# Performance work log

Measured on AMD Instinct MI355X. Metric: run time of the kernel, lower is better.

Reference implementation:

```python
import jax, jax.numpy as jnp
import numpy as np


def setup_inputs() -> dict:
    key = jax.random.key(0)
    kx, kw = jax.random.split(key)
    B, IN, OUT = 8192, 256, 16384
    x = jax.random.normal(kx, (B, IN), dtype=jnp.float32)
    weight = jax.random.normal(kw, (OUT, IN), dtype=jnp.float32)
    return {"x": x, "weight": weight}


def reference(x, weight):
    # Pairwise Euclidean distance ||x_b - w_o||_2 via expansion:
    temperature = 2.0
    x2 = jnp.sum(x * x, axis=1, keepdims=True)          # [B, 1]
    w2 = jnp.sum(weight * weight, axis=1)[None, :]       # [1, OUT]
    xw = x @ weight.T                                    # [B, OUT]
    d2 = jnp.maximum(x2 + w2 - 2.0 * xw, 0.0)            # clamp fp error
    dist = jnp.sqrt(d2)                                  # [B, OUT]
    return jax.nn.softmax(-temperature * dist, axis=1)
```

## Files before the change

kernel.cpp:

```cpp
#include <hip/hip_runtime.h>
#include <math.h>
#include <stdint.h>

#define M_ROWS 8192
#define N_COLS 16384
#define K_DIM  256
#define NTILE  (N_COLS / 128)
#define CHUNK  2048
#define NCHUNK 4

typedef _Float16 half8  __attribute__((ext_vector_type(8)));
typedef _Float16 half4v __attribute__((ext_vector_type(4)));
typedef float    vf4    __attribute__((ext_vector_type(4)));

__device__ __forceinline__ void gload16(const void* g, void* lds) {
  __builtin_amdgcn_global_load_lds(
      (__attribute__((address_space(1))) void*)(void*)g,
      (__attribute__((address_space(3))) void*)lds, 16, 0, 0);
}

__global__ __launch_bounds__(256) void prep_kernel(
    const float* __restrict__ x, const float* __restrict__ w,
    float* __restrict__ x2, float* __restrict__ w2,
    _Float16* __restrict__ xh, _Float16* __restrict__ wh) {
  int row  = blockIdx.x * 4 + (threadIdx.x >> 6);
  int lane = threadIdx.x & 63;
  const float* src; _Float16* dst; float* nrm;
  if (row < M_ROWS) {
    src = x + (size_t)row * K_DIM; dst = xh + (size_t)row * K_DIM; nrm = x2 + row;
  } else {
    int r = row - M_ROWS;
    src = w + (size_t)r * K_DIM; dst = wh + (size_t)r * K_DIM; nrm = w2 + r;
  }
  float4 v = ((const float4*)src)[lane];
  float s = v.x*v.x + v.y*v.y + v.z*v.z + v.w*v.w;
  #pragma unroll
  for (int off = 32; off > 0; off >>= 1) s += __shfl_down(s, off);
  if (lane == 0) *nrm = s;
  half4v h; h[0]=(_Float16)v.x; h[1]=(_Float16)v.y; h[2]=(_Float16)v.z; h[3]=(_Float16)v.w;
  ((half4v*)dst)[lane] = h;
}

template <int MODE>
__global__ __launch_bounds__(256, 3) void gemm_pass(
    const _Float16* __restrict__ A, const _Float16* __restrict__ Bm,
    const float* __restrict__ x2g, const float* __restrict__ w2g,
    const float* __restrict__ invg,
    float* __restrict__ partials,
    float* __restrict__ out) {
  __shared__ _Float16 As[128 * 64];
  __shared__ _Float16 Bs[128 * 64];
  __shared__ float x2s[128];
  __shared__ float w2s[128];
  __shared__ float invs[128];
  __shared__ float rowpart[2][128];

  int id   = blockIdx.x;
  int xcd  = id & 7;
  int rest = id >> 3;
  int ct   = xcd * 16 + (rest & 15);
  int rt   = rest >> 4;
  int brow = rt * 128;
  int bcol = ct * 128;

  int tid = threadIdx.x, lane = tid & 63, wid = tid >> 6;
  int wr = wid >> 1, wc = wid & 1;

  if (tid < 128) {
    x2s[tid] = x2g[brow + tid];
    if (MODE == 1) invs[tid] = invg[brow + tid];
  } else {
    w2s[tid - 128] = w2g[bcol + tid - 128];
  }

  vf4 acc[4][4] = {};

  for (int kk = 0; kk < K_DIM; kk += 64) {
    #pragma unroll
    for (int i = 0; i < 4; ++i) {
      int seg = wid * 4 + i;
      int r   = seg * 8 + (lane >> 3);
      int colhalf = ((lane & 7) * 8) ^ ((lane >> 3) << 3);
      gload16(A  + (size_t)(brow + r) * K_DIM + kk + colhalf, (char*)As + seg * 1024);
      gload16(Bm + (size_t)(bcol + r) * K_DIM + kk + colhalf, (char*)Bs + seg * 1024);
    }
    __syncthreads();

    #pragma unroll
    for (int ks = 0; ks < 2; ++ks) {
      half8 af[4], bf[4];
      int cb = ks * 64 + (lane >> 4) * 16;
      #pragma unroll
      for (int m = 0; m < 4; ++m) {
        int ra = wr * 64 + m * 16 + (lane & 15);
        af[m] = *(const half8*)((const char*)As + ra * 128 + (cb ^ ((ra & 7) << 4)));
      }
      #pragma unroll
      for (int n = 0; n < 4; ++n) {
        int rb = wc * 64 + n * 16 + (lane & 15);
        bf[n] = *(const half8*)((const char*)Bs + rb * 128 + (cb ^ ((rb & 7) << 4)));
      }
      #pragma unroll
      for (int m = 0; m < 4; ++m)
        #pragma unroll
        for (int n = 0; n < 4; ++n)
          acc[m][n] = __builtin_amdgcn_mfma_f32_16x16x32_f16(af[m], bf[n], acc[m][n], 0, 0, 0);
    }
    __syncthreads();
  }

  if (MODE == 0) {
    #pragma unroll
    for (int m = 0; m < 4; ++m) {
      #pragma unroll
      for (int j = 0; j < 4; ++j) {
        int rl = wr * 64 + m * 16 + ((lane >> 4) << 2) + j;
        float x2v = x2s[rl];
        float sm = 0.f;
        #pragma unroll
        for (int n = 0; n < 4; ++n) {
          int cl = wc * 64 + n * 16 + (lane & 15);
          float d2 = fmaxf(x2v + w2s[cl] - 2.0f * acc[m][n][j], 0.0f);
          sm += __expf(-2.0f * sqrtf(d2));
        }
        sm += __shfl_xor(sm, 1);
        sm += __shfl_xor(sm, 2);
        sm += __shfl_xor(sm, 4);
        sm += __shfl_xor(sm, 8);
        if ((lane & 15) == 0) rowpart[wc][rl] = sm;
      }
    }
    __syncthreads();
    if (tid < 128)
      partials[(size_t)(brow + tid) * NTILE + ct] = rowpart[0][tid] + rowpart[1][tid];
  } else {
    #pragma unroll
    for (int m = 0; m < 4; ++m) {
      #pragma unroll
      for (int j = 0; j < 4; ++j) {
        int rl = wr * 64 + m * 16 + ((lane >> 4) << 2) + j;
        float x2v = x2s[rl];
        float inv = invs[rl];
        size_t rowbase = (size_t)(brow + rl) * N_COLS + bcol;
        #pragma unroll
        for (int n = 0; n < 4; ++n) {
          int cl = wc * 64 + n * 16 + (lane & 15);
          float d2 = fmaxf(x2v + w2s[cl] - 2.0f * acc[m][n][j], 0.0f);
          out[rowbase + cl] = __expf(-2.0f * sqrtf(d2)) * inv;
        }
      }
    }
  }
}

__global__ __launch_bounds__(256) void reduce_inv(
    const float* __restrict__ partials, float* __restrict__ invg) {
  int row  = blockIdx.x * 4 + (threadIdx.x >> 6);
  int lane = threadIdx.x & 63;
  const float* p = partials + (size_t)row * NTILE;
  float s = p[lane] + p[lane + 64];
  #pragma unroll
  for (int off = 32; off > 0; off >>= 1) s += __shfl_down(s, off);
  if (lane == 0) invg[row] = 1.0f / s;
}

__global__ __launch_bounds__(256, 2) void gemm_logit_f32(
    const float* __restrict__ xf, const float* __restrict__ wf,
    float* __restrict__ out, int mbase) {
  __shared__ _Float16 As[128 * 64];
  __shared__ _Float16 Bs[128 * 64];
  __shared__ float x2s[128];
  __shared__ float w2s[128];

  int id  = blockIdx.x;
  int xcd = id & 7;
  int rt  = (id >> 3) & 15;
  int c2  = id >> 7;
  int brow = mbase + rt * 128;
  int bcol = (xcd * 16 + c2) * 128;

  int tid = threadIdx.x, lane = tid & 63, wid = tid >> 6;
  int wr = wid >> 1, wc = wid & 1;

  vf4 acc[4][4] = {};

  {
    const float* src = (tid < 128) ? xf + (size_t)(brow + tid) * K_DIM
                                   : wf + (size_t)(bcol + tid - 128) * K_DIM;
    float s = 0.f;
    for (int i = 0; i < 64; ++i) {
      float4 v = ((const float4*)src)[i];
      s += v.x*v.x + v.y*v.y + v.z*v.z + v.w*v.w;
    }
    if (tid < 128) x2s[tid] = s; else w2s[tid - 128] = s;
  }

  for (int kk = 0; kk < K_DIM; kk += 64) {
    #pragma unroll
    for (int i = 0; i < 8; ++i) {
      int idx = i * 256 + tid;
      int r = idx >> 4, kq = idx & 15;
      float4 va = ((const float4*)(xf + (size_t)(brow + r) * K_DIM + kk))[kq];
      float4 vb = ((const float4*)(wf + (size_t)(bcol + r) * K_DIM + kk))[kq];
      half4v ha; ha[0]=(_Float16)va.x; ha[1]=(_Float16)va.y; ha[2]=(_Float16)va.z; ha[3]=(_Float16)va.w;
      half4v hb; hb[0]=(_Float16)vb.x; hb[1]=(_Float16)vb.y; hb[2]=(_Float16)vb.z; hb[3]=(_Float16)vb.w;
      *(half4v*)&As[r * 64 + kq * 4] = ha;
      *(half4v*)&Bs[r * 64 + kq * 4] = hb;
    }
    __syncthreads();
    #pragma unroll
    for (int ks = 0; ks < 2; ++ks) {
      half8 af[4], bf[4];
      #pragma unroll
      for (int m = 0; m < 4; ++m)
        af[m] = *(const half8*)&As[(wr*64 + m*16 + (lane & 15)) * 64 + ks*32 + (lane >> 4) * 8];
      #pragma unroll
      for (int n = 0; n < 4; ++n)
        bf[n] = *(const half8*)&Bs[(wc*64 + n*16 + (lane & 15)) * 64 + ks*32 + (lane >> 4) * 8];
      #pragma unroll
      for (int m = 0; m < 4; ++m)
        #pragma unroll
        for (int n = 0; n < 4; ++n)
          acc[m][n] = __builtin_amdgcn_mfma_f32_16x16x32_f16(af[m], bf[n], acc[m][n], 0, 0, 0);
    }
    __syncthreads();
  }

  #pragma unroll
  for (int m = 0; m < 4; ++m) {
    int rl = wr * 64 + m * 16 + ((lane >> 4) << 2);
    #pragma unroll
    for (int n = 0; n < 4; ++n) {
      int cl = wc * 64 + n * 16 + (lane & 15);
      int c  = bcol + cl;
      float w2v = w2s[cl];
      #pragma unroll
      for (int j = 0; j < 4; ++j) {
        int r = brow + rl + j;
        float d2 = fmaxf(x2s[rl + j] + w2v - 2.0f * acc[m][n][j], 0.0f);
        out[(size_t)r * N_COLS + c] = -2.0f * sqrtf(d2);
      }
    }
  }
}

__global__ __launch_bounds__(256) void softmax_norm(float* __restrict__ io, int mbase) {
  int row = mbase + blockIdx.x;
  float* p = io + (size_t)row * N_COLS;
  int tid = threadIdx.x;
  __shared__ float wsum[4];

  float4 v[16];
  float s = 0.f;
  #pragma unroll
  for (int i = 0; i < 16; ++i) {
    v[i] = ((const float4*)p)[i * 256 + tid];
    v[i].x = __expf(v[i].x); v[i].y = __expf(v[i].y);
    v[i].z = __expf(v[i].z); v[i].w = __expf(v[i].w);
    s += v[i].x + v[i].y + v[i].z + v[i].w;
  }
  #pragma unroll
  for (int off = 32; off > 0; off >>= 1) s += __shfl_down(s, off);
  if ((tid & 63) == 0) wsum[tid >> 6] = s;
  __syncthreads();
  float inv = 1.0f / (wsum[0] + wsum[1] + wsum[2] + wsum[3]);
  #pragma unroll
  for (int i = 0; i < 16; ++i) {
    float4 o = v[i];
    o.x *= inv; o.y *= inv; o.z *= inv; o.w *= inv;
    ((float4*)p)[i * 256 + tid] = o;
  }
}

extern "C" void kernel_launch(void* const* d_in, const int* in_sizes, int n_in,
                              void* d_out, int out_size, void* d_ws, size_t ws_size,
                              hipStream_t stream) {
  const float* x = (const float*)d_in[0];
  const float* w = (const float*)d_in[1];
  float* out = (float*)d_out;

  char* ws = (char*)d_ws;
  float* x2 = (float*)ws;
  float* w2 = x2 + M_ROWS;
  float* invsum = w2 + N_COLS;
  float* partials = invsum + M_ROWS;
  _Float16* xh = (_Float16*)(partials + (size_t)M_ROWS * NTILE);
  _Float16* wh = xh + (size_t)M_ROWS * K_DIM;
  const size_t need = ((size_t)(M_ROWS + N_COLS + M_ROWS) + (size_t)M_ROWS * NTILE) * 4
                    + (size_t)(M_ROWS + N_COLS) * K_DIM * 2;

  if (ws_size >= need) {
    prep_kernel<<<(M_ROWS + N_COLS) / 4, 256, 0, stream>>>(x, w, x2, w2, xh, wh);
    gemm_pass<0><<<(M_ROWS / 128) * (N_COLS / 128), 256, 0, stream>>>(
        xh, wh, x2, w2, nullptr, partials, nullptr);
    reduce_inv<<<M_ROWS / 4, 256, 0, stream>>>(partials, invsum);
    gemm_pass<1><<<(M_ROWS / 128) * (N_COLS / 128), 256, 0, stream>>>(
        xh, wh, x2, w2, invsum, nullptr, out);
  } else {
    for (int c = 0; c < NCHUNK; ++c) {
      int mbase = c * CHUNK;
      gemm_logit_f32<<<(CHUNK / 128) * (N_COLS / 128), 256, 0, stream>>>(
          x, w, out, mbase);
      softmax_norm<<<CHUNK, 256, 0, stream>>>(out, mbase);
    }
  }
}
```

Baseline: 311.0 us.

## Pre-pack fp16 operands into MFMA fragment order and load directly to registers

The prep kernel now writes x and weight in fp16, arranged in 16-row by 32-k fragment blocks that match the MFMA operand layout. Each lane of the GEMM kernels can then load its half8 fragment straight from global memory, so the LDS staging, swizzling and __syncthreads barriers go away. The norms and inverse sums are also read from global memory instead of being staged in shared memory. The cost is that fragments are no longer shared through LDS, so each wave issues its own global loads and data reuse relies on L1/L2 caching.

```diff
diff --git a/kernel.cpp b/kernel.cpp
--- a/kernel.cpp
+++ b/kernel.cpp
@@ -13,46 +13,45 @@
 typedef _Float16 half4v __attribute__((ext_vector_type(4)));
 typedef float    vf4    __attribute__((ext_vector_type(4)));
 
-__device__ __forceinline__ void gload16(const void* g, void* lds) {
-  __builtin_amdgcn_global_load_lds(
-      (__attribute__((address_space(1))) void*)(void*)g,
-      (__attribute__((address_space(3))) void*)lds, 16, 0, 0);
-}
-
-__global__ __launch_bounds__(256) void prep_kernel(
+__global__ __launch_bounds__(256) void prep_pack(
     const float* __restrict__ x, const float* __restrict__ w,
     float* __restrict__ x2, float* __restrict__ w2,
-    _Float16* __restrict__ xh, _Float16* __restrict__ wh) {
-  int row  = blockIdx.x * 4 + (threadIdx.x >> 6);
+    _Float16* __restrict__ xp, _Float16* __restrict__ wp) {
+  int g    = blockIdx.x * 4 + (threadIdx.x >> 6);
   int lane = threadIdx.x & 63;
   const float* src; _Float16* dst; float* nrm;
-  if (row < M_ROWS) {
-    src = x + (size_t)row * K_DIM; dst = xh + (size_t)row * K_DIM; nrm = x2 + row;
+  if (g < M_ROWS / 16) {
+    src = x + (size_t)g * 16 * K_DIM; dst = xp + (size_t)g * 8 * 512; nrm = x2 + g * 16;
   } else {
-    int r = row - M_ROWS;
-    src = w + (size_t)r * K_DIM; dst = wh + (size_t)r * K_DIM; nrm = w2 + r;
-  }
-  float4 v = ((const float4*)src)[lane];
-  float s = v.x*v.x + v.y*v.y + v.z*v.z + v.w*v.w;
-  #pragma unroll
-  for (int off = 32; off > 0; off >>= 1) s += __shfl_down(s, off);
-  if (lane == 0) *nrm = s;
-  half4v h; h[0]=(_Float16)v.x; h[1]=(_Float16)v.y; h[2]=(_Float16)v.z; h[3]=(_Float16)v.w;
-  ((half4v*)dst)[lane] = h;
+    int g2 = g - M_ROWS / 16;
+    src = w + (size_t)g2 * 16 * K_DIM; dst = wp + (size_t)g2 * 8 * 512; nrm = w2 + g2 * 16;
+  }
+  int rowl = lane & 15, kpart = lane >> 4;
+  float ss = 0.f;
+  #pragma unroll
+  for (int S = 0; S < 8; ++S) {
+    const float* p = src + rowl * K_DIM + S * 32 + kpart * 8;
+    float4 a = *(const float4*)p;
+    float4 b = *(const float4*)(p + 4);
+    ss += a.x*a.x + a.y*a.y + a.z*a.z + a.w*a.w
+        + b.x*b.x + b.y*b.y + b.z*b.z + b.w*b.w;
+    half8 h;
+    h[0]=(_Float16)a.x; h[1]=(_Float16)a.y; h[2]=(_Float16)a.z; h[3]=(_Float16)a.w;
+    h[4]=(_Float16)b.x; h[5]=(_Float16)b.y; h[6]=(_Float16)b.z; h[7]=(_Float16)b.w;
+    *(half8*)(dst + S * 512 + lane * 8) = h;
+  }
+  ss += __shfl_xor(ss, 16);
+  ss += __shfl_xor(ss, 32);
+  if (lane < 16) nrm[lane] = ss;
 }
 
 template <int MODE>
 __global__ __launch_bounds__(256, 3) void gemm_pass(
-    const _Float16* __restrict__ A, const _Float16* __restrict__ Bm,
+    const _Float16* __restrict__ Ap, const _Float16* __restrict__ Bp,
     const float* __restrict__ x2g, const float* __restrict__ w2g,
     const float* __restrict__ invg,
     float* __restrict__ partials,
     float* __restrict__ out) {
-  __shared__ _Float16 As[128 * 64];
-  __shared__ _Float16 Bs[128 * 64];
-  __shared__ float x2s[128];
-  __shared__ float w2s[128];
-  __shared__ float invs[128];
   __shared__ float rowpart[2][128];
 
   int id   = blockIdx.x;
@@ -66,47 +65,25 @@
   int tid = threadIdx.x, lane = tid & 63, wid = tid >> 6;
   int wr = wid >> 1, wc = wid & 1;
 
-  if (tid < 128) {
-    x2s[tid] = x2g[brow + tid];
-    if (MODE == 1) invs[tid] = invg[brow + tid];
-  } else {
-    w2s[tid - 128] = w2g[bcol + tid - 128];
-  }
+  int RA = rt * 8 + wr * 4;
+  int RB = ct * 8 + wc * 4;
 
   vf4 acc[4][4] = {};
 
-  for (int kk = 0; kk < K_DIM; kk += 64) {
-    #pragma unroll
-    for (int i = 0; i < 4; ++i) {
-      int seg = wid * 4 + i;
-      int r   = seg * 8 + (lane >> 3);
-      int colhalf = ((lane & 7) * 8) ^ ((lane >> 3) << 3);
-      gload16(A  + (size_t)(brow + r) * K_DIM + kk + colhalf, (char*)As + seg * 1024);
-      gload16(Bm + (size_t)(bcol + r) * K_DIM + kk + colhalf, (char*)Bs + seg * 1024);
-    }
-    __syncthreads();
-
-    #pragma unroll
-    for (int ks = 0; ks < 2; ++ks) {
-      half8 af[4], bf[4];
-      int cb = ks * 64 + (lane >> 4) * 16;
-      #pragma unroll
-      for (int m = 0; m < 4; ++m) {
-        int ra = wr * 64 + m * 16 + (lane & 15);
-        af[m] = *(const half8*)((const char*)As + ra * 128 + (cb ^ ((ra & 7) << 4)));
-      }
-      #pragma unroll
-      for (int n = 0; n < 4; ++n) {
-        int rb = wc * 64 + n * 16 + (lane & 15);
-        bf[n] = *(const half8*)((const char*)Bs + rb * 128 + (cb ^ ((rb & 7) << 4)));
-      }
-      #pragma unroll
-      for (int m = 0; m < 4; ++m)
-        #pragma unroll
-        for (int n = 0; n < 4; ++n)
-          acc[m][n] = __builtin_amdgcn_mfma_f32_16x16x32_f16(af[m], bf[n], acc[m][n], 0, 0, 0);
-    }
-    __syncthreads();
+  #pragma unroll
+  for (int S = 0; S < 8; ++S) {
+    half8 af[4], bf[4];
+    #pragma unroll
+    for (int m = 0; m < 4; ++m)
+      af[m] = *(const half8*)(Ap + (((size_t)(RA + m) * 8 + S) << 9) + lane * 8);
+    #pragma unroll
+    for (int n = 0; n < 4; ++n)
+      bf[n] = *(const half8*)(Bp + (((size_t)(RB + n) * 8 + S) << 9) + lane * 8);
+    #pragma unroll
+    for (int m = 0; m < 4; ++m)
+      #pragma unroll
+      for (int n = 0; n < 4; ++n)
+        acc[m][n] = __builtin_amdgcn_mfma_f32_16x16x32_f16(af[m], bf[n], acc[m][n], 0, 0, 0);
   }
 
   if (MODE == 0) {
@@ -115,12 +92,12 @@
       #pragma unroll
       for (int j = 0; j < 4; ++j) {
         int rl = wr * 64 + m * 16 + ((lane >> 4) << 2) + j;
-        float x2v = x2s[rl];
+        float x2v = x2g[brow + rl];
         float sm = 0.f;
         #pragma unroll
         for (int n = 0; n < 4; ++n) {
           int cl = wc * 64 + n * 16 + (lane & 15);
-          float d2 = fmaxf(x2v + w2s[cl] - 2.0f * acc[m][n][j], 0.0f);
+          float d2 = fmaxf(x2v + w2g[bcol + cl] - 2.0f * acc[m][n][j], 0.0f);
           sm += __expf(-2.0f * sqrtf(d2));
         }
         sm += __shfl_xor(sm, 1);
@@ -139,13 +116,13 @@
       #pragma unroll
       for (int j = 0; j < 4; ++j) {
         int rl = wr * 64 + m * 16 + ((lane >> 4) << 2) + j;
-        float x2v = x2s[rl];
-        float inv = invs[rl];
+        float x2v = x2g[brow + rl];
+        float inv = invg[brow + rl];
         size_t rowbase = (size_t)(brow + rl) * N_COLS + bcol;
         #pragma unroll
         for (int n = 0; n < 4; ++n) {
           int cl = wc * 64 + n * 16 + (lane & 15);
-          float d2 = fmaxf(x2v + w2s[cl] - 2.0f * acc[m][n][j], 0.0f);
+          float d2 = fmaxf(x2v + w2g[bcol + cl] - 2.0f * acc[m][n][j], 0.0f);
           out[rowbase + cl] = __expf(-2.0f * sqrtf(d2)) * inv;
         }
       }
@@ -284,18 +261,18 @@
   float* w2 = x2 + M_ROWS;
   float* invsum = w2 + N_COLS;
   float* partials = invsum + M_ROWS;
-  _Float16* xh = (_Float16*)(partials + (size_t)M_ROWS * NTILE);
-  _Float16* wh = xh + (size_t)M_ROWS * K_DIM;
+  _Float16* xp = (_Float16*)(partials + (size_t)M_ROWS * NTILE);
+  _Float16* wp = xp + (size_t)M_ROWS * K_DIM;
   const size_t need = ((size_t)(M_ROWS + N_COLS + M_ROWS) + (size_t)M_ROWS * NTILE) * 4
                     + (size_t)(M_ROWS + N_COLS) * K_DIM * 2;
 
   if (ws_size >= need) {
-    prep_kernel<<<(M_ROWS + N_COLS) / 4, 256, 0, stream>>>(x, w, x2, w2, xh, wh);
+    prep_pack<<<(M_ROWS + N_COLS) / 16 / 4, 256, 0, stream>>>(x, w, x2, w2, xp, wp);
     gemm_pass<0><<<(M_ROWS / 128) * (N_COLS / 128), 256, 0, stream>>>(
-        xh, wh, x2, w2, nullptr, partials, nullptr);
+        xp, wp, x2, w2, nullptr, partials, nullptr);
     reduce_inv<<<M_ROWS / 4, 256, 0, stream>>>(partials, invsum);
     gemm_pass<1><<<(M_ROWS / 128) * (N_COLS / 128), 256, 0, stream>>>(
-        xh, wh, x2, w2, invsum, nullptr, out);
+        xp, wp, x2, w2, invsum, nullptr, out);
   } else {
     for (int c = 0; c < NCHUNK; ++c) {
       int mbase = c * CHUNK;
```

Result: slower. 384.3 us (+23.6%).

## Replace double GEMM pass with single GEMM storing fp16 dot products per chunk

Applied to the files above, without the earlier changes.

Instead of running the GEMM twice (once for row sums, once for output), each 2048-row chunk now runs the GEMM once. It writes fp16 dot products to a workspace buffer along with per-tile exp partial sums, then reduces and runs a streaming finalize kernel that recomputes distances and writes normalized outputs. This trades recomputed MFMA work for extra memory traffic through the intermediate buffer, which chunking may keep cache-resident. The old fp32 fallback path is removed.

```diff
diff --git a/kernel.cpp b/kernel.cpp
--- a/kernel.cpp
+++ b/kernel.cpp
@@ -6,8 +6,8 @@
 #define N_COLS 16384
 #define K_DIM  256
 #define NTILE  (N_COLS / 128)
-#define CHUNK  2048
-#define NCHUNK 4
+#define CROWS  2048
+#define NCHUNK (M_ROWS / CROWS)
 
 typedef _Float16 half8  __attribute__((ext_vector_type(8)));
 typedef _Float16 half4v __attribute__((ext_vector_type(4)));
@@ -39,6 +39,136 @@
   if (lane == 0) *nrm = s;
   half4v h; h[0]=(_Float16)v.x; h[1]=(_Float16)v.y; h[2]=(_Float16)v.z; h[3]=(_Float16)v.w;
   ((half4v*)dst)[lane] = h;
+}
+
+__global__ __launch_bounds__(256, 3) void gemm_xw(
+    const _Float16* __restrict__ A, const _Float16* __restrict__ Bm,
+    const float* __restrict__ x2g, const float* __restrict__ w2g,
+    float* __restrict__ partials, _Float16* __restrict__ xwc, int mbase) {
+  __shared__ _Float16 As[128 * 64];
+  __shared__ _Float16 Bs[128 * 64];
+  __shared__ float x2s[128];
+  __shared__ float w2s[128];
+  __shared__ float rowpart[2][128];
+
+  int id   = blockIdx.x;
+  int xcd  = id & 7;
+  int rest = id >> 3;
+  int ct   = xcd * 16 + (rest & 15);
+  int rt   = rest >> 4;
+  int browl = rt * 128;
+  int brow  = mbase + browl;
+  int bcol  = ct * 128;
+
+  int tid = threadIdx.x, lane = tid & 63, wid = tid >> 6;
+  int wr = wid >> 1, wc = wid & 1;
+
+  if (tid < 128) x2s[tid] = x2g[brow + tid];
+  else           w2s[tid - 128] = w2g[bcol + tid - 128];
+
+  vf4 acc[4][4] = {};
+
+  for (int kk = 0; kk < K_DIM; kk += 64) {
+    #pragma unroll
+    for (int i = 0; i < 4; ++i) {
+      int seg = wid * 4 + i;
+      int r   = seg * 8 + (lane >> 3);
+      int colhalf = ((lane & 7) * 8) ^ ((lane >> 3) << 3);
+      gload16(A  + (size_t)(brow + r) * K_DIM + kk + colhalf, (char*)As + seg * 1024);
+      gload16(Bm + (size_t)(bcol + r) * K_DIM + kk + colhalf, (char*)Bs + seg * 1024);
+    }
+    __syncthreads();
+
+    #pragma unroll
+    for (int ks = 0; ks < 2; ++ks) {
+      half8 af[4], bf[4];
+      int cb = ks * 64 + (lane >> 4) * 16;
+      #pragma unroll
+      for (int m = 0; m < 4; ++m) {
+        int ra = wr * 64 + m * 16 + (lane & 15);
+        af[m] = *(const half8*)((const char*)As + ra * 128 + (cb ^ ((ra & 7) << 4)));
+      }
+      #pragma unroll
+      for (int n = 0; n < 4; ++n) {
+        int rb = wc * 64 + n * 16 + (lane & 15);
+        bf[n] = *(const half8*)((const char*)Bs + rb * 128 + (cb ^ ((rb & 7) << 4)));
+      }
+      #pragma unroll
+      for (int m = 0; m < 4; ++m)
+        #pragma unroll
+        for (int n = 0; n < 4; ++n)
+          acc[m][n] = __builtin_amdgcn_mfma_f32_16x16x32_f16(af[m], bf[n], acc[m][n], 0, 0, 0);
+    }
+    __syncthreads();
+  }
+
+  #pragma unroll
+  for (int m = 0; m < 4; ++m) {
+    #pragma unroll
+    for (int j = 0; j < 4; ++j) {
+      int rl = wr * 64 + m * 16 + ((lane >> 4) << 2) + j;
+      float x2v = x2s[rl];
+      size_t rowbase = (size_t)(browl + rl) * N_COLS + bcol;
+      float sm = 0.f;
+      #pragma unroll
+      for (int n = 0; n < 4; ++n) {
+        int cl = wc * 64 + n * 16 + (lane & 15);
+        float xwv = acc[m][n][j];
+        float d2 = fmaxf(x2v + w2s[cl] - 2.0f * xwv, 0.0f);
+        sm += __expf(-2.0f * sqrtf(d2));
+        xwc[rowbase + cl] = (_Float16)xwv;
+      }
+      sm += __shfl_xor(sm, 1);
+      sm += __shfl_xor(sm, 2);
+      sm += __shfl_xor(sm, 4);
+      sm += __shfl_xor(sm, 8);
+      if ((lane & 15) == 0) rowpart[wc][rl] = sm;
+    }
+  }
+  __syncthreads();
+  if (tid < 128)
+    partials[(size_t)(brow + tid) * NTILE + ct] = rowpart[0][tid] + rowpart[1][tid];
+}
+
+__global__ __launch_bounds__(256) void reduce_inv(
+    const float* __restrict__ partials, float* __restrict__ invg, int mbase) {
+  int row  = mbase + blockIdx.x * 4 + (threadIdx.x >> 6);
+  int lane = threadIdx.x & 63;
+  const float* p = partials + (size_t)row * NTILE;
+  float s = p[lane] + p[lane + 64];
+  #pragma unroll
+  for (int off = 32; off > 0; off >>= 1) s += __shfl_down(s, off);
+  if (lane == 0) invg[row] = 1.0f / s;
+}
+
+__global__ __launch_bounds__(256) void finalize_kernel(
+    const _Float16* __restrict__ xwc, const float* __restrict__ x2g,
+    const float* __restrict__ w2g, const float* __restrict__ invg,
+    float* __restrict__ out, int mbase) {
+  const size_t NV = (size_t)CROWS * N_COLS / 8;
+  size_t stride = (size_t)gridDim.x * blockDim.x;
+  float* outc = out + (size_t)mbase * N_COLS;
+  for (size_t i = (size_t)blockIdx.x * blockDim.x + threadIdx.x; i < NV; i += stride) {
+    size_t base = i * 8;
+    int rowl = (int)(base >> 14);
+    int col  = (int)(base & (N_COLS - 1));
+    half8 h = *(const half8*)(xwc + base);
+    float x2v = x2g[mbase + rowl];
+    float inv = invg[mbase + rowl];
+    float4 wa = *(const float4*)(w2g + col);
+    float4 wb = *(const float4*)(w2g + col + 4);
+    float4 o0, o1;
+    o0.x = __expf(-2.f * sqrtf(fmaxf(x2v + wa.x - 2.f * (float)h[0], 0.f))) * inv;
+    o0.y = __expf(-2.f * sqrtf(fmaxf(x2v + wa.y - 2.f * (float)h[1], 0.f))) * inv;
+    o0.z = __expf(-2.f * sqrtf(fmaxf(x2v + wa.z - 2.f * (float)h[2], 0.f))) * inv;
+    o0.w = __expf(-2.f * sqrtf(fmaxf(x2v + wa.w - 2.f * (float)h[3], 0.f))) * inv;
+    o1.x = __expf(-2.f * sqrtf(fmaxf(x2v + wb.x - 2.f * (float)h[4], 0.f))) * inv;
+    o1.y = __expf(-2.f * sqrtf(fmaxf(x2v + wb.y - 2.f * (float)h[5], 0.f))) * inv;
+    o1.z = __expf(-2.f * sqrtf(fmaxf(x2v + wb.z - 2.f * (float)h[6], 0.f))) * inv;
+    o1.w = __expf(-2.f * sqrtf(fmaxf(x2v + wb.w - 2.f * (float)h[7], 0.f))) * inv;
+    *(float4*)(outc + base)     = o0;
+    *(float4*)(outc + base + 4) = o1;
+  }
 }
 
 template <int MODE>
@@ -85,7 +215,6 @@
       gload16(Bm + (size_t)(bcol + r) * K_DIM + kk + colhalf, (char*)Bs + seg * 1024);
     }
     __syncthreads();
-
     #pragma unroll
     for (int ks = 0; ks < 2; ++ks) {
       half8 af[4], bf[4];
@@ -153,7 +282,7 @@
   }
 }
 
-__global__ __launch_bounds__(256) void reduce_inv(
+__global__ __launch_bounds__(256) void reduce_inv_full(
     const float* __restrict__ partials, float* __restrict__ invg) {
   int row  = blockIdx.x * 4 + (threadIdx.x >> 6);
   int lane = threadIdx.x & 63;
@@ -164,114 +293,6 @@
   if (lane == 0) invg[row] = 1.0f / s;
 }
 
-__global__ __launch_bounds__(256, 2) void gemm_logit_f32(
-    const float* __restrict__ xf, const float* __restrict__ wf,
-    float* __restrict__ out, int mbase) {
-  __shared__ _Float16 As[128 * 64];
-  __shared__ _Float16 Bs[128 * 64];
-  __shared__ float x2s[128];
-  __shared__ float w2s[128];
-
-  int id  = blockIdx.x;
-  int xcd = id & 7;
-  int rt  = (id >> 3) & 15;
-  int c2  = id >> 7;
-  int brow = mbase + rt * 128;
-  int bcol = (xcd * 16 + c2) * 128;
-
-  int tid = threadIdx.x, lane = tid & 63, wid = tid >> 6;
-  int wr = wid >> 1, wc = wid & 1;
-
-  vf4 acc[4][4] = {};
-
-  {
-    const float* src = (tid < 128) ? xf + (size_t)(brow + tid) * K_DIM
-                                   : wf + (size_t)(bcol + tid - 128) * K_DIM;
-    float s = 0.f;
-    for (int i = 0; i < 64; ++i) {
-      float4 v = ((const float4*)src)[i];
-      s += v.x*v.x + v.y*v.y + v.z*v.z + v.w*v.w;
-    }
-    if (tid < 128) x2s[tid] = s; else w2s[tid - 128] = s;
-  }
-
-  for (int kk = 0; kk < K_DIM; kk += 64) {
-    #pragma unroll
-    for (int i = 0; i < 8; ++i) {
-      int idx = i * 256 + tid;
-      int r = idx >> 4, kq = idx & 15;
-      float4 va = ((const float4*)(xf + (size_t)(brow + r) * K_DIM + kk))[kq];
-      float4 vb = ((const float4*)(wf + (size_t)(bcol + r) * K_DIM + kk))[kq];
-      half4v ha; ha[0]=(_Float16)va.x; ha[1]=(_Float16)va.y; ha[2]=(_Float16)va.z; ha[3]=(_Float16)va.w;
-      half4v hb; hb[0]=(_Float16)vb.x; hb[1]=(_Float16)vb.y; hb[2]=(_Float16)vb.z; hb[3]=(_Float16)vb.w;
-      *(half4v*)&As[r * 64 + kq * 4] = ha;
-      *(half4v*)&Bs[r * 64 + kq * 4] = hb;
-    }
-    __syncthreads();
-    #pragma unroll
-    for (int ks = 0; ks < 2; ++ks) {
-      half8 af[4], bf[4];
-      #pragma unroll
-      for (int m = 0; m < 4; ++m)
-        af[m] = *(const half8*)&As[(wr*64 + m*16 + (lane & 15)) * 64 + ks*32 + (lane >> 4) * 8];
-      #pragma unroll
-      for (int n = 0; n < 4; ++n)
-        bf[n] = *(const half8*)&Bs[(wc*64 + n*16 + (lane & 15)) * 64 + ks*32 + (lane >> 4) * 8];
-      #pragma unroll
-      for (int m = 0; m < 4; ++m)
-        #pragma unroll
-        for (int n = 0; n < 4; ++n)
-          acc[m][n] = __builtin_amdgcn_mfma_f32_16x16x32_f16(af[m], bf[n], acc[m][n], 0, 0, 0);
-    }
-    __syncthreads();
-  }
-
-  #pragma unroll
-  for (int m = 0; m < 4; ++m) {
-    int rl = wr * 64 + m * 16 + ((lane >> 4) << 2);
-    #pragma unroll
-    for (int n = 0; n < 4; ++n) {
-      int cl = wc * 64 + n * 16 + (lane & 15);
-      int c  = bcol + cl;
-      float w2v = w2s[cl];
-      #pragma unroll
-      for (int j = 0; j < 4; ++j) {
-        int r = brow + rl + j;
-        float d2 = fmaxf(x2s[rl + j] + w2v - 2.0f * acc[m][n][j], 0.0f);
-        out[(size_t)r * N_COLS + c] = -2.0f * sqrtf(d2);
-      }
-    }
-  }
-}
-
-__global__ __launch_bounds__(256) void softmax_norm(float* __restrict__ io, int mbase) {
-  int row = mbase + blockIdx.x;
-  float* p = io + (size_t)row * N_COLS;
-  int tid = threadIdx.x;
-  __shared__ float wsum[4];
-
-  float4 v[16];
-  float s = 0.f;
-  #pragma unroll
-  for (int i = 0; i < 16; ++i) {
-    v[i] = ((const float4*)p)[i * 256 + tid];
-    v[i].x = __expf(v[i].x); v[i].y = __expf(v[i].y);
-    v[i].z = __expf(v[i].z); v[i].w = __expf(v[i].w);
-    s += v[i].x + v[i].y + v[i].z + v[i].w;
-  }
-  #pragma unroll
-  for (int off = 32; off > 0; off >>= 1) s += __shfl_down(s, off);
-  if ((tid & 63) == 0) wsum[tid >> 6] = s;
-  __syncthreads();
-  float inv = 1.0f / (wsum[0] + wsum[1] + wsum[2] + wsum[3]);
-  #pragma unroll
-  for (int i = 0; i < 16; ++i) {
-    float4 o = v[i];
-    o.x *= inv; o.y *= inv; o.z *= inv; o.w *= inv;
-    ((float4*)p)[i * 256 + tid] = o;
-  }
-}
-
 extern "C" void kernel_launch(void* const* d_in, const int* in_sizes, int n_in,
                               void* d_out, int out_size, void* d_ws, size_t ws_size,
                               hipStream_t stream) {
@@ -286,22 +307,26 @@
   float* partials = invsum + M_ROWS;
   _Float16* xh = (_Float16*)(partials + (size_t)M_ROWS * NTILE);
   _Float16* wh = xh + (size_t)M_ROWS * K_DIM;
-  const size_t need = ((size_t)(M_ROWS + N_COLS + M_ROWS) + (size_t)M_ROWS * NTILE) * 4
-                    + (size_t)(M_ROWS + N_COLS) * K_DIM * 2;
-
-  if (ws_size >= need) {
+  _Float16* xwc = wh + (size_t)N_COLS * K_DIM;
+  const size_t needB = ((size_t)(M_ROWS + N_COLS + M_ROWS) + (size_t)M_ROWS * NTILE) * 4
+                     + (size_t)(M_ROWS + N_COLS) * K_DIM * 2;
+  const size_t needA = needB + (size_t)CROWS * N_COLS * 2;
+
+  if (ws_size >= needA) {
+    prep_kernel<<<(M_ROWS + N_COLS) / 4, 256, 0, stream>>>(x, w, x2, w2, xh, wh);
+    for (int c = 0; c < NCHUNK; ++c) {
+      int mbase = c * CROWS;
+      gemm_xw<<<(CROWS / 128) * (N_COLS / 128), 256, 0, stream>>>(
+          xh, wh, x2, w2, partials, xwc, mbase);
+      reduce_inv<<<CROWS / 4, 256, 0, stream>>>(partials, invsum, mbase);
+      finalize_kernel<<<2048, 256, 0, stream>>>(xwc, x2, w2, invsum, out, mbase);
+    }
+  } else if (ws_size >= needB) {
     prep_kernel<<<(M_ROWS + N_COLS) / 4, 256, 0, stream>>>(x, w, x2, w2, xh, wh);
     gemm_pass<0><<<(M_ROWS / 128) * (N_COLS / 128), 256, 0, stream>>>(
         xh, wh, x2, w2, nullptr, partials, nullptr);
-    reduce_inv<<<M_ROWS / 4, 256, 0, stream>>>(partials, invsum);
+    reduce_inv_full<<<M_ROWS / 4, 256, 0, stream>>>(partials, invsum);
     gemm_pass<1><<<(M_ROWS / 128) * (N_COLS / 128), 256, 0, stream>>>(
         xh, wh, x2, w2, invsum, nullptr, out);
-  } else {
-    for (int c = 0; c < NCHUNK; ++c) {
-      int mbase = c * CHUNK;
-      gemm_logit_f32<<<(CHUNK / 128) * (N_COLS / 128), 256, 0, stream>>>(
-          x, w, out, mbase);
-      softmax_norm<<<CHUNK, 256, 0, stream>>>(out, mbase);
-    }
-  }
-}
+  }
+}
```

Measured after the change: 336.0 us. 1.08x slower.
